# Kernel tuning notes

Hardware: AMD Instinct MI355X
Metric: run time of the kernel (lower is better)

The kernel has to match this reference:

```python
import jax, jax.numpy as jnp
import numpy as np

B, T, I, H = 32, 2048, 64, 512
OS_FACTOR = 2.0
K = 1.0 / OS_FACTOR  # Euler step size


def setup_inputs() -> dict:
    key = jax.random.key(0)
    k0, k1, k2, k3, k4 = jax.random.split(key, 5)
    x = jax.random.normal(k0, (B, T, I), dtype=jnp.float32)
    # LSTMCell parameters: gate order [i, f, g, o], shapes match torch.nn.LSTMCell
    W_ih = jax.random.normal(k1, (4 * H, I), dtype=jnp.float32) * 0.05
    W_hh = jax.random.normal(k2, (4 * H, H), dtype=jnp.float32) * 0.05
    b_ih = jax.random.normal(k3, (4 * H,), dtype=jnp.float32) * 0.05
    b_hh = jax.random.normal(k4, (4 * H,), dtype=jnp.float32) * 0.05
    return {"x": x, "W_ih": W_ih, "W_hh": W_hh, "b_ih": b_ih, "b_hh": b_hh}


def _lstm_cell(xt, hh, cc, W_ih, W_hh, b_ih, b_hh):
    # torch.nn.LSTMCell math, gate order i, f, g, o
    gates = xt @ W_ih.T + b_ih + hh @ W_hh.T + b_hh  # [B, 4H]
    i, f, g, o = jnp.split(gates, 4, axis=-1)
    c_new = jax.nn.sigmoid(f) * cc + jax.nn.sigmoid(i) * jnp.tanh(g)
    h_new = jax.nn.sigmoid(o) * jnp.tanh(c_new)
    return h_new, c_new


def _forward(x, W_ih, W_hh, b_ih, b_hh):
    # STNRNN simple-Euler: h <- h + k * (cell(x_i, h) - h), state vec = [h | c]
    h0 = jnp.zeros((x.shape[0], 2 * H), dtype=x.dtype)

    def step(hstate, xt):
        hh, cc = hstate[:, :H], hstate[:, H:]
        h_new, c_new = _lstm_cell(xt, hh, cc, W_ih, W_hh, b_ih, b_hh)
        hc = jnp.concatenate([h_new, c_new], axis=-1)  # tuple_to_vector
        h_next = hstate + K * (hc - hstate)            # Euler update
        return h_next, h_next

    h_final, states = jax.lax.scan(step, h0, jnp.swapaxes(x, 0, 1))  # states: [T, B, 2H]
    states = jnp.swapaxes(states, 0, 1)  # [B, T, 2H]
    return states[..., :H], h_final


def reference(x, W_ih, W_hh, b_ih, b_hh):
    return _forward(x, W_ih, W_hh, b_ih, b_hh)
```

## Files before the change

### kernel.cpp

```cpp
#include <hip/hip_runtime.h>
#include <hip/hip_bf16.h>
#include <stdint.h>
#include <stddef.h>


#define T_STEPS 2048
#define H_DIM   512
#define I_DIM   64
#define B_TOT   32
#define NGROUP  16
#define WGS     16
#define BPG     2
#define NTH     256

typedef float f32x4 __attribute__((ext_vector_type(4)));
typedef short s16x8 __attribute__((ext_vector_type(8)));

#define STATE_HALF (B_TOT*H_DIM)
#define SHI_BYTES  (2*STATE_HALF*2)
#define SRES_OFF   SHI_BYTES
#define CNT_OFF    (SRES_OFF + SHI_BYTES)
#define WS_BYTES   (CNT_OFF + NGROUP*T_STEPS*4)

__device__ __forceinline__ unsigned short bf16_rne(float f) {
  __hip_bfloat16 b = __float2bfloat16(f);
  return __builtin_bit_cast(unsigned short, b);
}
__device__ __forceinline__ float bf16_to_f(unsigned short u) {
  return __uint_as_float(((unsigned)u) << 16);
}
__device__ __forceinline__ f32x4 ld_agent_b128(const void* p) {
  f32x4 r;
  asm volatile("global_load_dwordx4 %0, %1, off sc0 sc1" : "=v"(r) : "v"(p));
  return r;
}
__device__ __forceinline__ void st_agent_u16(void* p, unsigned v) {
  asm volatile("global_store_short %0, %1, off sc0 sc1" :: "v"(p), "v"(v) : "memory");
}
__device__ __forceinline__ s16x8 make_frag(const float* p) {
  const float4 a = *(const float4*)p;
  const float4 b = *(const float4*)(p + 4);
  s16x8 f;
  f[0] = (short)bf16_rne(a.x); f[1] = (short)bf16_rne(a.y);
  f[2] = (short)bf16_rne(a.z); f[3] = (short)bf16_rne(a.w);
  f[4] = (short)bf16_rne(b.x); f[5] = (short)bf16_rne(b.y);
  f[6] = (short)bf16_rne(b.z); f[7] = (short)bf16_rne(b.w);
  return f;
}
__device__ __forceinline__ void split8(const float4& a, const float4& b,
                                       s16x8& hi, s16x8& lo) {
  float v[8] = {a.x, a.y, a.z, a.w, b.x, b.y, b.z, b.w};
  #pragma unroll
  for (int e = 0; e < 8; ++e) {
    const unsigned short h = bf16_rne(v[e]);
    hi[e] = (short)h;
    lo[e] = (short)bf16_rne(v[e] - bf16_to_f(h));
  }
}
__device__ __forceinline__ float sigmoid_f(float v) { return 1.0f / (1.0f + __expf(-v)); }
__device__ __forceinline__ float tanh_f(float v)    { return 1.0f - 2.0f / (1.0f + __expf(2.0f * v)); }

extern "C" __global__ void __launch_bounds__(NTH, 1)
stnrnn_kernel(const float* __restrict__ x,
              const float* __restrict__ Wih,
              const float* __restrict__ Whh,
              const float* __restrict__ bih,
              const float* __restrict__ bhh,
              float* __restrict__ out,
              unsigned short* sHi,
              unsigned short* sRes,
              int* cnt)
{
  const int bid = blockIdx.x;
  const int g   = bid & 15;
  const int m   = bid >> 4;
  const int tid = threadIdx.x;
  const int w   = tid >> 6;
  const int l   = tid & 63;
  const int p   = l >> 4;
  const int c16 = l & 15;
  const int bb  = c16 & 1;
  const int bg0 = g * BPG;
  const int jj  = c16 >> 2, q = c16 & 3;

  s16x8 ahh[2][16];
  s16x8 aih[2][2];
  #pragma unroll
  for (int rt = 0; rt < 2; ++rt) {
    const int jbase = m * 32 + (w * 2 + rt) * 4;
    const int grow  = q * H_DIM + jbase + jj;
    #pragma unroll
    for (int kt = 0; kt < 16; ++kt)
      ahh[rt][kt] = make_frag(Whh + (size_t)grow * H_DIM + kt * 32 + p * 8);
    #pragma unroll
    for (int kt = 0; kt < 2; ++kt)
      aih[rt][kt] = make_frag(Wih + (size_t)grow * I_DIM + kt * 32 + p * 8);
  }
  float bias[2][4];
  #pragma unroll
  for (int rt = 0; rt < 2; ++rt) {
    const int jme = m * 32 + (w * 2 + rt) * 4 + p;
    #pragma unroll
    for (int qq = 0; qq < 4; ++qq)
      bias[rt][qq] = bih[qq * H_DIM + jme] + bhh[qq * H_DIM + jme];
  }
  const int  jme[2]  = {m * 32 + (w * 2) * 4 + p, m * 32 + (w * 2 + 1) * 4 + p};
  const int  bme     = bg0 + c16;
  const bool active  = (c16 < BPG);

  float hreg[2] = {0.f, 0.f}, creg[2] = {0.f, 0.f};
  int* const mycnt = cnt + g * T_STEPS;

  for (int t = 0; t < T_STEPS; ++t) {
    const float* xp = x + ((size_t)(bg0 + bb) * T_STEPS + t) * I_DIM + p * 8;
    const float4 xv0a = *(const float4*)(xp);
    const float4 xv0b = *(const float4*)(xp + 4);
    const float4 xv1a = *(const float4*)(xp + 32);
    const float4 xv1b = *(const float4*)(xp + 32 + 4);

    const unsigned short* hiB = sHi  + (size_t)(t & 1) * STATE_HALF;
    const unsigned short* reB = sRes + (size_t)(t & 1) * STATE_HALF;
    const size_t bOff = (size_t)(bg0 + bb) * H_DIM + p * 8;
    f32x4 bhi[16], bres[16];
    #pragma unroll
    for (int kt = 0; kt < 16; ++kt) {
      bhi[kt]  = ld_agent_b128(hiB + bOff + kt * 32);
      bres[kt] = ld_agent_b128(reB + bOff + kt * 32);
    }

    f32x4 acc[2] = {{0.f, 0.f, 0.f, 0.f}, {0.f, 0.f, 0.f, 0.f}};

    asm volatile("s_waitcnt vmcnt(20)" ::: "memory");
    __builtin_amdgcn_sched_barrier(0);
    #pragma unroll
    for (int kt = 0; kt < 8; ++kt) {
      const s16x8 bh = __builtin_bit_cast(s16x8, bhi[kt]);
      const s16x8 br = __builtin_bit_cast(s16x8, bres[kt]);
      acc[0] = __builtin_amdgcn_mfma_f32_16x16x32_bf16(ahh[0][kt], bh, acc[0], 0, 0, 0);
      acc[1] = __builtin_amdgcn_mfma_f32_16x16x32_bf16(ahh[1][kt], bh, acc[1], 0, 0, 0);
      acc[0] = __builtin_amdgcn_mfma_f32_16x16x32_bf16(ahh[0][kt], br, acc[0], 0, 0, 0);
      acc[1] = __builtin_amdgcn_mfma_f32_16x16x32_bf16(ahh[1][kt], br, acc[1], 0, 0, 0);
    }
    asm volatile("s_waitcnt vmcnt(0)" ::: "memory");
    __builtin_amdgcn_sched_barrier(0);
    #pragma unroll
    for (int kt = 8; kt < 16; ++kt) {
      const s16x8 bh = __builtin_bit_cast(s16x8, bhi[kt]);
      const s16x8 br = __builtin_bit_cast(s16x8, bres[kt]);
      acc[0] = __builtin_amdgcn_mfma_f32_16x16x32_bf16(ahh[0][kt], bh, acc[0], 0, 0, 0);
      acc[1] = __builtin_amdgcn_mfma_f32_16x16x32_bf16(ahh[1][kt], bh, acc[1], 0, 0, 0);
      acc[0] = __builtin_amdgcn_mfma_f32_16x16x32_bf16(ahh[0][kt], br, acc[0], 0, 0, 0);
      acc[1] = __builtin_amdgcn_mfma_f32_16x16x32_bf16(ahh[1][kt], br, acc[1], 0, 0, 0);
    }
    {
      s16x8 xh0, xr0, xh1, xr1;
      split8(xv0a, xv0b, xh0, xr0);
      split8(xv1a, xv1b, xh1, xr1);
      acc[0] = __builtin_amdgcn_mfma_f32_16x16x32_bf16(aih[0][0], xh0, acc[0], 0, 0, 0);
      acc[1] = __builtin_amdgcn_mfma_f32_16x16x32_bf16(aih[1][0], xh0, acc[1], 0, 0, 0);
      acc[0] = __builtin_amdgcn_mfma_f32_16x16x32_bf16(aih[0][0], xr0, acc[0], 0, 0, 0);
      acc[1] = __builtin_amdgcn_mfma_f32_16x16x32_bf16(aih[1][0], xr0, acc[1], 0, 0, 0);
      acc[0] = __builtin_amdgcn_mfma_f32_16x16x32_bf16(aih[0][1], xh1, acc[0], 0, 0, 0);
      acc[1] = __builtin_amdgcn_mfma_f32_16x16x32_bf16(aih[1][1], xh1, acc[1], 0, 0, 0);
      acc[0] = __builtin_amdgcn_mfma_f32_16x16x32_bf16(aih[0][1], xr1, acc[0], 0, 0, 0);
      acc[1] = __builtin_amdgcn_mfma_f32_16x16x32_bf16(aih[1][1], xr1, acc[1], 0, 0, 0);
    }

    if (active) {
      unsigned short* oHi = sHi  + (size_t)((t + 1) & 1) * STATE_HALF + (size_t)bme * H_DIM;
      unsigned short* oRe = sRes + (size_t)((t + 1) & 1) * STATE_HALF + (size_t)bme * H_DIM;
      #pragma unroll
      for (int rt = 0; rt < 2; ++rt) {
        const float gi = acc[rt][0] + bias[rt][0];
        const float gf = acc[rt][1] + bias[rt][1];
        const float gg = acc[rt][2] + bias[rt][2];
        const float go = acc[rt][3] + bias[rt][3];
        const float si = sigmoid_f(gi);
        const float sf = sigmoid_f(gf);
        const float so = sigmoid_f(go);
        const float cn = sf * creg[rt] + si * tanh_f(gg);
        const float hn = so * tanh_f(cn);
        const float hs = 0.5f * (hreg[rt] + hn);
        const float cs = 0.5f * (creg[rt] + cn);
        hreg[rt] = hs; creg[rt] = cs;
        out[((size_t)bme * T_STEPS + t) * H_DIM + jme[rt]] = hs;
        const unsigned short h16 = bf16_rne(hs);
        const unsigned short r16 = bf16_rne(hs - bf16_to_f(h16));
        st_agent_u16(oHi + jme[rt], h16);
        st_agent_u16(oRe + jme[rt], r16);
        if (t == T_STEPS - 1) {
          const size_t base2 = (size_t)B_TOT * T_STEPS * H_DIM;
          out[base2 + (size_t)bme * 1024 + jme[rt]] = hs;
          out[base2 + (size_t)bme * 1024 + H_DIM + jme[rt]] = cs;
        }
      }
    }

    if (t < T_STEPS - 1) {
      asm volatile("s_waitcnt vmcnt(0)" ::: "memory");
      __syncthreads();
      if (tid == 0) {
        __hip_atomic_fetch_add(mycnt + t, 1, __ATOMIC_RELAXED,
                               __HIP_MEMORY_SCOPE_AGENT);
        while (__hip_atomic_load(mycnt + t, __ATOMIC_RELAXED,
                                 __HIP_MEMORY_SCOPE_AGENT) < WGS)
          __builtin_amdgcn_s_sleep(1);
        asm volatile("" ::: "memory");
      }
      __syncthreads();
    }
  }
}

extern "C" void kernel_launch(void* const* d_in, const int* in_sizes, int n_in,
                              void* d_out, int out_size, void* d_ws, size_t ws_size,
                              hipStream_t stream) {
  (void)in_sizes; (void)n_in; (void)out_size; (void)ws_size;
  const float* x   = (const float*)d_in[0];
  const float* Wih = (const float*)d_in[1];
  const float* Whh = (const float*)d_in[2];
  const float* bih = (const float*)d_in[3];
  const float* bhh = (const float*)d_in[4];
  float* out = (float*)d_out;
  unsigned short* sHi  = (unsigned short*)d_ws;
  unsigned short* sRes = (unsigned short*)((char*)d_ws + SRES_OFF);
  int* cnt = (int*)((char*)d_ws + CNT_OFF);

  hipMemsetAsync(d_ws, 0, WS_BYTES, stream);

  hipLaunchKernelGGL(stnrnn_kernel, dim3(NGROUP * WGS), dim3(NTH), 0,
                     stream, x, Wih, Whh, bih, bhh, out, sHi, sRes, cnt);
}
```

Baseline: 11.25 ms.

## Replace per-step atomic group barrier with per-wave flag polling

Drops the per-step workgroup barrier, which used __syncthreads plus an atomic counter. Instead, each wave publishes a monotonically increasing step flag and polls all 64 flags of its batch group before loading the shared hidden state. The input-projection MFMAs are hoisted ahead of the wait so they overlap the synchronization latency. The recurrent MFMAs are also spread across four independent accumulator chains for more instruction-level parallelism. In exchange, every wave issues 16 coherent flag loads per poll, which adds memory traffic.

```diff
diff --git a/kernel.cpp b/kernel.cpp
--- a/kernel.cpp
+++ b/kernel.cpp
@@ -19,8 +19,8 @@
 #define STATE_HALF (B_TOT*H_DIM)
 #define SHI_BYTES  (2*STATE_HALF*2)
 #define SRES_OFF   SHI_BYTES
-#define CNT_OFF    (SRES_OFF + SHI_BYTES)
-#define WS_BYTES   (CNT_OFF + NGROUP*T_STEPS*4)
+#define FLAGS_OFF  (2*SHI_BYTES)
+#define WS_BYTES   (FLAGS_OFF + NGROUP*64*4)
 
 __device__ __forceinline__ unsigned short bf16_rne(float f) {
   __hip_bfloat16 b = __float2bfloat16(f);
@@ -29,13 +29,21 @@
 __device__ __forceinline__ float bf16_to_f(unsigned short u) {
   return __uint_as_float(((unsigned)u) << 16);
 }
-__device__ __forceinline__ f32x4 ld_agent_b128(const void* p) {
+__device__ __forceinline__ f32x4 ld_mall_b128(const void* p) {
   f32x4 r;
   asm volatile("global_load_dwordx4 %0, %1, off sc0 sc1" : "=v"(r) : "v"(p));
   return r;
 }
-__device__ __forceinline__ void st_agent_u16(void* p, unsigned v) {
+__device__ __forceinline__ uint4 ld_mall_u4(const void* p) {
+  uint4 r;
+  asm volatile("global_load_dwordx4 %0, %1, off sc0 sc1" : "=v"(r) : "v"(p));
+  return r;
+}
+__device__ __forceinline__ void st_mall_u16(void* p, unsigned v) {
   asm volatile("global_store_short %0, %1, off sc0 sc1" :: "v"(p), "v"(v) : "memory");
+}
+__device__ __forceinline__ void st_mall_b32(void* p, unsigned v) {
+  asm volatile("global_store_dword %0, %1, off sc0 sc1" :: "v"(p), "v"(v) : "memory");
 }
 __device__ __forceinline__ s16x8 make_frag(const float* p) {
   const float4 a = *(const float4*)p;
@@ -69,7 +77,7 @@
               float* __restrict__ out,
               unsigned short* sHi,
               unsigned short* sRes,
-              int* cnt)
+              unsigned* flags)
 {
   const int bid = blockIdx.x;
   const int g   = bid & 15;
@@ -99,76 +107,116 @@
   float bias[2][4];
   #pragma unroll
   for (int rt = 0; rt < 2; ++rt) {
-    const int jme = m * 32 + (w * 2 + rt) * 4 + p;
+    const int jx = m * 32 + (w * 2 + rt) * 4 + p;
     #pragma unroll
     for (int qq = 0; qq < 4; ++qq)
-      bias[rt][qq] = bih[qq * H_DIM + jme] + bhh[qq * H_DIM + jme];
-  }
-  const int  jme[2]  = {m * 32 + (w * 2) * 4 + p, m * 32 + (w * 2 + 1) * 4 + p};
-  const int  bme     = bg0 + c16;
-  const bool active  = (c16 < BPG);
+      bias[rt][qq] = bih[qq * H_DIM + jx] + bhh[qq * H_DIM + jx];
+  }
+  const int  jme[2] = {m * 32 + (w * 2) * 4 + p, m * 32 + (w * 2 + 1) * 4 + p};
+  const int  bme    = bg0 + c16;
+  const bool active = (c16 < BPG);
 
   float hreg[2] = {0.f, 0.f}, creg[2] = {0.f, 0.f};
-  int* const mycnt = cnt + g * T_STEPS;
+  const unsigned* const gflags = flags + g * 64;
+  unsigned* const myflag = flags + g * 64 + m * 4 + w;
 
   for (int t = 0; t < T_STEPS; ++t) {
-    const float* xp = x + ((size_t)(bg0 + bb) * T_STEPS + t) * I_DIM + p * 8;
-    const float4 xv0a = *(const float4*)(xp);
-    const float4 xv0b = *(const float4*)(xp + 4);
-    const float4 xv1a = *(const float4*)(xp + 32);
-    const float4 xv1b = *(const float4*)(xp + 32 + 4);
-
     const unsigned short* hiB = sHi  + (size_t)(t & 1) * STATE_HALF;
     const unsigned short* reB = sRes + (size_t)(t & 1) * STATE_HALF;
-    const size_t bOff = (size_t)(bg0 + bb) * H_DIM + p * 8;
-    f32x4 bhi[16], bres[16];
-    #pragma unroll
-    for (int kt = 0; kt < 16; ++kt) {
-      bhi[kt]  = ld_agent_b128(hiB + bOff + kt * 32);
-      bres[kt] = ld_agent_b128(reB + bOff + kt * 32);
-    }
-
-    f32x4 acc[2] = {{0.f, 0.f, 0.f, 0.f}, {0.f, 0.f, 0.f, 0.f}};
-
-    asm volatile("s_waitcnt vmcnt(20)" ::: "memory");
-    __builtin_amdgcn_sched_barrier(0);
-    #pragma unroll
-    for (int kt = 0; kt < 8; ++kt) {
-      const s16x8 bh = __builtin_bit_cast(s16x8, bhi[kt]);
-      const s16x8 br = __builtin_bit_cast(s16x8, bres[kt]);
-      acc[0] = __builtin_amdgcn_mfma_f32_16x16x32_bf16(ahh[0][kt], bh, acc[0], 0, 0, 0);
-      acc[1] = __builtin_amdgcn_mfma_f32_16x16x32_bf16(ahh[1][kt], bh, acc[1], 0, 0, 0);
-      acc[0] = __builtin_amdgcn_mfma_f32_16x16x32_bf16(ahh[0][kt], br, acc[0], 0, 0, 0);
-      acc[1] = __builtin_amdgcn_mfma_f32_16x16x32_bf16(ahh[1][kt], br, acc[1], 0, 0, 0);
-    }
-    asm volatile("s_waitcnt vmcnt(0)" ::: "memory");
-    __builtin_amdgcn_sched_barrier(0);
-    #pragma unroll
-    for (int kt = 8; kt < 16; ++kt) {
-      const s16x8 bh = __builtin_bit_cast(s16x8, bhi[kt]);
-      const s16x8 br = __builtin_bit_cast(s16x8, bres[kt]);
-      acc[0] = __builtin_amdgcn_mfma_f32_16x16x32_bf16(ahh[0][kt], bh, acc[0], 0, 0, 0);
-      acc[1] = __builtin_amdgcn_mfma_f32_16x16x32_bf16(ahh[1][kt], bh, acc[1], 0, 0, 0);
-      acc[0] = __builtin_amdgcn_mfma_f32_16x16x32_bf16(ahh[0][kt], br, acc[0], 0, 0, 0);
-      acc[1] = __builtin_amdgcn_mfma_f32_16x16x32_bf16(ahh[1][kt], br, acc[1], 0, 0, 0);
-    }
+    unsigned short* oHiBase = sHi  + (size_t)((t + 1) & 1) * STATE_HALF;
+    unsigned short* oReBase = sRes + (size_t)((t + 1) & 1) * STATE_HALF;
+
+    f32x4 a0 = {0.f,0.f,0.f,0.f}, a1 = {0.f,0.f,0.f,0.f};
+    f32x4 a2 = {0.f,0.f,0.f,0.f}, a3 = {0.f,0.f,0.f,0.f};
+
     {
+      const float* xp = x + ((size_t)(bg0 + bb) * T_STEPS + t) * I_DIM + p * 8;
+      const float4 xv0a = *(const float4*)(xp);
+      const float4 xv0b = *(const float4*)(xp + 4);
+      const float4 xv1a = *(const float4*)(xp + 32);
+      const float4 xv1b = *(const float4*)(xp + 36);
       s16x8 xh0, xr0, xh1, xr1;
       split8(xv0a, xv0b, xh0, xr0);
       split8(xv1a, xv1b, xh1, xr1);
-      acc[0] = __builtin_amdgcn_mfma_f32_16x16x32_bf16(aih[0][0], xh0, acc[0], 0, 0, 0);
-      acc[1] = __builtin_amdgcn_mfma_f32_16x16x32_bf16(aih[1][0], xh0, acc[1], 0, 0, 0);
-      acc[0] = __builtin_amdgcn_mfma_f32_16x16x32_bf16(aih[0][0], xr0, acc[0], 0, 0, 0);
-      acc[1] = __builtin_amdgcn_mfma_f32_16x16x32_bf16(aih[1][0], xr0, acc[1], 0, 0, 0);
-      acc[0] = __builtin_amdgcn_mfma_f32_16x16x32_bf16(aih[0][1], xh1, acc[0], 0, 0, 0);
-      acc[1] = __builtin_amdgcn_mfma_f32_16x16x32_bf16(aih[1][1], xh1, acc[1], 0, 0, 0);
-      acc[0] = __builtin_amdgcn_mfma_f32_16x16x32_bf16(aih[0][1], xr1, acc[0], 0, 0, 0);
-      acc[1] = __builtin_amdgcn_mfma_f32_16x16x32_bf16(aih[1][1], xr1, acc[1], 0, 0, 0);
-    }
+      a0 = __builtin_amdgcn_mfma_f32_16x16x32_bf16(aih[0][0], xh0, a0, 0, 0, 0);
+      a0 = __builtin_amdgcn_mfma_f32_16x16x32_bf16(aih[0][0], xr0, a0, 0, 0, 0);
+      a2 = __builtin_amdgcn_mfma_f32_16x16x32_bf16(aih[1][0], xh0, a2, 0, 0, 0);
+      a2 = __builtin_amdgcn_mfma_f32_16x16x32_bf16(aih[1][0], xr0, a2, 0, 0, 0);
+      a1 = __builtin_amdgcn_mfma_f32_16x16x32_bf16(aih[0][1], xh1, a1, 0, 0, 0);
+      a1 = __builtin_amdgcn_mfma_f32_16x16x32_bf16(aih[0][1], xr1, a1, 0, 0, 0);
+      a3 = __builtin_amdgcn_mfma_f32_16x16x32_bf16(aih[1][1], xh1, a3, 0, 0, 0);
+      a3 = __builtin_amdgcn_mfma_f32_16x16x32_bf16(aih[1][1], xr1, a3, 0, 0, 0);
+    }
+
+    if (t > 0) {
+      const unsigned tgt = (unsigned)t;
+      for (;;) {
+        uint4 f[16];
+        #pragma unroll
+        for (int i = 0; i < 16; ++i) f[i] = ld_mall_u4(gflags + i * 4);
+        asm volatile("s_waitcnt vmcnt(0)" ::: "memory");
+        __builtin_amdgcn_sched_barrier(0);
+        unsigned mn = 0xffffffffu;
+        #pragma unroll
+        for (int i = 0; i < 16; ++i) {
+          mn = f[i].x < mn ? f[i].x : mn;
+          mn = f[i].y < mn ? f[i].y : mn;
+          mn = f[i].z < mn ? f[i].z : mn;
+          mn = f[i].w < mn ? f[i].w : mn;
+        }
+        if (mn >= tgt) break;
+        __builtin_amdgcn_s_sleep(1);
+      }
+      __builtin_amdgcn_sched_barrier(0);
+    }
+
+    const size_t bOff = (size_t)(bg0 + bb) * H_DIM + p * 8;
+    f32x4 bhi[16], bres[16];
+    #pragma unroll
+    for (int kt = 0; kt < 16; ++kt) {
+      bhi[kt]  = ld_mall_b128(hiB + bOff + kt * 32);
+      bres[kt] = ld_mall_b128(reB + bOff + kt * 32);
+    }
+
+    asm volatile("s_waitcnt vmcnt(16)" ::: "memory");
+    __builtin_amdgcn_sched_barrier(0);
+    #pragma unroll
+    for (int kt = 0; kt < 8; kt += 2) {
+      const s16x8 vh = __builtin_bit_cast(s16x8, bhi[kt]);
+      const s16x8 vr = __builtin_bit_cast(s16x8, bres[kt]);
+      a0 = __builtin_amdgcn_mfma_f32_16x16x32_bf16(ahh[0][kt], vh, a0, 0, 0, 0);
+      a0 = __builtin_amdgcn_mfma_f32_16x16x32_bf16(ahh[0][kt], vr, a0, 0, 0, 0);
+      a2 = __builtin_amdgcn_mfma_f32_16x16x32_bf16(ahh[1][kt], vh, a2, 0, 0, 0);
+      a2 = __builtin_amdgcn_mfma_f32_16x16x32_bf16(ahh[1][kt], vr, a2, 0, 0, 0);
+      const s16x8 wh = __builtin_bit_cast(s16x8, bhi[kt + 1]);
+      const s16x8 wr = __builtin_bit_cast(s16x8, bres[kt + 1]);
+      a1 = __builtin_amdgcn_mfma_f32_16x16x32_bf16(ahh[0][kt + 1], wh, a1, 0, 0, 0);
+      a1 = __builtin_amdgcn_mfma_f32_16x16x32_bf16(ahh[0][kt + 1], wr, a1, 0, 0, 0);
+      a3 = __builtin_amdgcn_mfma_f32_16x16x32_bf16(ahh[1][kt + 1], wh, a3, 0, 0, 0);
+      a3 = __builtin_amdgcn_mfma_f32_16x16x32_bf16(ahh[1][kt + 1], wr, a3, 0, 0, 0);
+    }
+    asm volatile("s_waitcnt vmcnt(0)" ::: "memory");
+    __builtin_amdgcn_sched_barrier(0);
+    #pragma unroll
+    for (int kt = 8; kt < 16; kt += 2) {
+      const s16x8 vh = __builtin_bit_cast(s16x8, bhi[kt]);
+      const s16x8 vr = __builtin_bit_cast(s16x8, bres[kt]);
+      a0 = __builtin_amdgcn_mfma_f32_16x16x32_bf16(ahh[0][kt], vh, a0, 0, 0, 0);
+      a0 = __builtin_amdgcn_mfma_f32_16x16x32_bf16(ahh[0][kt], vr, a0, 0, 0, 0);
+      a2 = __builtin_amdgcn_mfma_f32_16x16x32_bf16(ahh[1][kt], vh, a2, 0, 0, 0);
+      a2 = __builtin_amdgcn_mfma_f32_16x16x32_bf16(ahh[1][kt], vr, a2, 0, 0, 0);
+      const s16x8 wh = __builtin_bit_cast(s16x8, bhi[kt + 1]);
+      const s16x8 wr = __builtin_bit_cast(s16x8, bres[kt + 1]);
+      a1 = __builtin_amdgcn_mfma_f32_16x16x32_bf16(ahh[0][kt + 1], wh, a1, 0, 0, 0);
+      a1 = __builtin_amdgcn_mfma_f32_16x16x32_bf16(ahh[0][kt + 1], wr, a1, 0, 0, 0);
+      a3 = __builtin_amdgcn_mfma_f32_16x16x32_bf16(ahh[1][kt + 1], wh, a3, 0, 0, 0);
+      a3 = __builtin_amdgcn_mfma_f32_16x16x32_bf16(ahh[1][kt + 1], wr, a3, 0, 0, 0);
+    }
+    const f32x4 acc[2] = {a0 + a1, a2 + a3};
 
     if (active) {
-      unsigned short* oHi = sHi  + (size_t)((t + 1) & 1) * STATE_HALF + (size_t)bme * H_DIM;
-      unsigned short* oRe = sRes + (size_t)((t + 1) & 1) * STATE_HALF + (size_t)bme * H_DIM;
+      unsigned short* oHi = oHiBase + (size_t)bme * H_DIM;
+      unsigned short* oRe = oReBase + (size_t)bme * H_DIM;
       #pragma unroll
       for (int rt = 0; rt < 2; ++rt) {
         const float gi = acc[rt][0] + bias[rt][0];
@@ -186,8 +234,8 @@
         out[((size_t)bme * T_STEPS + t) * H_DIM + jme[rt]] = hs;
         const unsigned short h16 = bf16_rne(hs);
         const unsigned short r16 = bf16_rne(hs - bf16_to_f(h16));
-        st_agent_u16(oHi + jme[rt], h16);
-        st_agent_u16(oRe + jme[rt], r16);
+        st_mall_u16(oHi + jme[rt], h16);
+        st_mall_u16(oRe + jme[rt], r16);
         if (t == T_STEPS - 1) {
           const size_t base2 = (size_t)B_TOT * T_STEPS * H_DIM;
           out[base2 + (size_t)bme * 1024 + jme[rt]] = hs;
@@ -198,16 +246,8 @@
 
     if (t < T_STEPS - 1) {
       asm volatile("s_waitcnt vmcnt(0)" ::: "memory");
-      __syncthreads();
-      if (tid == 0) {
-        __hip_atomic_fetch_add(mycnt + t, 1, __ATOMIC_RELAXED,
-                               __HIP_MEMORY_SCOPE_AGENT);
-        while (__hip_atomic_load(mycnt + t, __ATOMIC_RELAXED,
-                                 __HIP_MEMORY_SCOPE_AGENT) < WGS)
-          __builtin_amdgcn_s_sleep(1);
-        asm volatile("" ::: "memory");
-      }
-      __syncthreads();
+      __builtin_amdgcn_sched_barrier(0);
+      if (l == 0) st_mall_b32(myflag, (unsigned)(t + 1));
     }
   }
 }
@@ -224,10 +264,10 @@
   float* out = (float*)d_out;
   unsigned short* sHi  = (unsigned short*)d_ws;
   unsigned short* sRes = (unsigned short*)((char*)d_ws + SRES_OFF);
-  int* cnt = (int*)((char*)d_ws + CNT_OFF);
+  unsigned* flags = (unsigned*)((char*)d_ws + FLAGS_OFF);
 
   hipMemsetAsync(d_ws, 0, WS_BYTES, stream);
 
   hipLaunchKernelGGL(stnrnn_kernel, dim3(NGROUP * WGS), dim3(NTH), 0,
-                     stream, x, Wih, Whh, bih, bhh, out, sHi, sRes, cnt);
-}
+                     stream, x, Wih, Whh, bih, bhh, out, sHi, sRes, flags);
+}
```

Measured after the change: 18.63 ms. 65.6% more time.
